# Kernel tuning notes

Hardware: AMD Instinct MI355X
Metric: run time of the kernel (lower is better)

Reference implementation:

```python
import jax, jax.numpy as jnp
import numpy as np
import math

NUM_HEADS = 12


def setup_inputs() -> dict:
    key = jax.random.key(0)
    ks = jax.random.split(key, 9)
    R, L, B, E = 128, 512, 1, 768
    s = 1.0 / math.sqrt(E)
    return {
        "x": jax.random.normal(ks[0], (R, L, B, E), dtype=jnp.float32),
        "wq": jax.random.normal(ks[1], (E, E), dtype=jnp.float32) * s,
        "bq": jax.random.normal(ks[2], (E,), dtype=jnp.float32) * 0.02,
        "wk": jax.random.normal(ks[3], (E, E), dtype=jnp.float32) * s,
        "bk": jax.random.normal(ks[4], (E,), dtype=jnp.float32) * 0.02,
        "wv": jax.random.normal(ks[5], (E, E), dtype=jnp.float32) * s,
        "bv": jax.random.normal(ks[6], (E,), dtype=jnp.float32) * 0.02,
        "wo": jax.random.normal(ks[7], (E, E), dtype=jnp.float32) * s,
        "bo": jax.random.normal(ks[8], (E,), dtype=jnp.float32) * 0.02,
    }


def reference(x, wq, bq, wk, bk, wv, bv, wo, bo):
    # x: [num_rows, num_cols, batch, embed_dim]
    R, L, B, E = x.shape
    H = NUM_HEADS
    D = E // H
    # scaling = head_dim**-0.5 / sqrt(num_rows)  (align_scaling)
    scaling = (D ** -0.5) / math.sqrt(R)

    q = (x @ wq.T + bq).reshape(R, L, B, H, D) * scaling
    k = (x @ wk.T + bk).reshape(R, L, B, H, D)
    v = (x @ wv.T + bv).reshape(R, L, B, H, D)

    # row attention: contract over rows r and head_dim d -> logits [h, n, i, j]
    attn_weights = jnp.einsum("rinhd,rjnhd->hnij", q, k)
    attn_probs = jax.nn.softmax(attn_weights, axis=-1)

    context = jnp.einsum("hnij,rjnhd->rinhd", attn_probs, v)
    context = context.reshape(R, L, B, E)
    output = context @ wo.T + bo
    return (output, attn_probs)
```

## Files before the change

kernel.cpp:

```cpp
#include <hip/hip_runtime.h>
#include <hip/hip_bf16.h>

typedef unsigned short u16;
typedef u16   u16x4 __attribute__((ext_vector_type(4)));
typedef u16   u16x8 __attribute__((ext_vector_type(8)));
typedef short bf16x8 __attribute__((ext_vector_type(8)));
typedef float f32x4 __attribute__((ext_vector_type(4)));

#define R_    128
#define L_    512
#define E_    768
#define H_    12
#define RD_   8192
#define M_    65536
#define OUT0_N 50331648
#define PART_ 3145728

__device__ __forceinline__ u16 rne_bf16(float f) {
  unsigned u = __builtin_bit_cast(unsigned, f);
  u += 0x7FFFu + ((u >> 16) & 1u);
  return (u16)(u >> 16);
}

__device__ __forceinline__ void gload_lds16(const u16* g, u16* l) {
  __builtin_amdgcn_global_load_lds(
      (const __attribute__((address_space(1))) void*)g,
      (__attribute__((address_space(3))) void*)l, 16, 0, 0);
}

__device__ __forceinline__ int xcd_remap(int d, int nwg) {
  return (d & 7) * (nwg >> 3) + (d >> 3);
}

__device__ __forceinline__ void gemm_core256(
    const u16* __restrict__ Ab, const u16* __restrict__ Bb,
    const int lda, const int ldb, const int K,
    u16* sm, f32x4 acc[8][4])
{
  const int t    = threadIdx.x;
  const int lane = t & 63;
  const int w    = t >> 6;
  const int wm   = (w >> 2) << 7;
  const int wn   = (w & 3) << 6;
  const int frow = lane & 15;

  const int srow  = t >> 2;
  const int gslot = (t & 3) ^ ((t >> 3) & 3);
  const u16* gA0 = Ab + (size_t)srow * lda + (gslot << 3);
  const u16* gA1 = Ab + (size_t)(srow + 128) * lda + (gslot << 3);
  const u16* gB0 = Bb + (size_t)srow * ldb + (gslot << 3);
  const u16* gB1 = Bb + (size_t)(srow + 128) * ldb + (gslot << 3);
  const int stg = t << 3;

  const int rdoff = (((lane >> 4) ^ ((lane >> 1) & 3)) << 3);

#define STAGE256(tt_, buf_)                                            \
  {                                                                    \
    const size_t ko_ = (size_t)(tt_) << 5;                             \
    gload_lds16(gA0 + ko_, (buf_) + stg);                              \
    gload_lds16(gA1 + ko_, (buf_) + 4096 + stg);                       \
    gload_lds16(gB0 + ko_, (buf_) + 8192 + stg);                       \
    gload_lds16(gB1 + ko_, (buf_) + 12288 + stg);                      \
  }

  const int nt = K >> 5;
  STAGE256(0, sm);
  if (nt > 1) STAGE256(1, sm + 16384);
  asm volatile("s_waitcnt vmcnt(4)" ::: "memory");
  __builtin_amdgcn_s_barrier();

  for (int tt = 0; tt < nt; ++tt) {
    u16* bufc = sm + (tt % 3) * 16384;
    const bool st = (tt + 2 < nt);
    if (st) STAGE256(tt + 2, sm + ((tt + 2) % 3) * 16384);

    bf16x8 af[8], bff[4];
#pragma unroll
    for (int b = 0; b < 4; ++b)
      bff[b] = *(const bf16x8*)(bufc + 8192 + ((wn + b * 16 + frow) << 5) + rdoff);
#pragma unroll
    for (int a = 0; a < 8; ++a)
      af[a] = *(const bf16x8*)(bufc + ((wm + a * 16 + frow) << 5) + rdoff);

    __builtin_amdgcn_s_setprio(1);
#pragma unroll
    for (int a = 0; a < 8; ++a)
#pragma unroll
      for (int b = 0; b < 4; ++b)
        acc[a][b] = __builtin_amdgcn_mfma_f32_16x16x32_bf16(af[a], bff[b], acc[a][b], 0, 0, 0);
    __builtin_amdgcn_s_setprio(0);

    if (st) asm volatile("s_waitcnt vmcnt(4)" ::: "memory");
    else    asm volatile("s_waitcnt vmcnt(0)" ::: "memory");
    __builtin_amdgcn_s_barrier();
  }
#undef STAGE256
}

#define EPILOGUE_IDX256                           \
  const int lane = threadIdx.x & 63;              \
  const int w    = threadIdx.x >> 6;              \
  const int wm   = (w >> 2) << 7;                 \
  const int wn   = (w & 3) << 6;                  \
  const int row4 = (lane >> 4) << 2;              \
  const int coll = lane & 15;

#define ACC_INIT256                               \
  f32x4 acc[8][4];                                \
  {                                               \
    f32x4 zz = {0.0f, 0.0f, 0.0f, 0.0f};          \
    _Pragma("unroll")                             \
    for (int a = 0; a < 8; ++a)                   \
      _Pragma("unroll")                           \
      for (int b = 0; b < 4; ++b) acc[a][b] = zz; \
  }

__device__ __forceinline__ void gemm_core(
    const u16* __restrict__ Ab, const u16* __restrict__ Bb,
    const int lda, const int ldb, const int K,
    u16* sm, f32x4 acc[4][4])
{
  const int t    = threadIdx.x;
  const int lane = t & 63;
  const int w    = t >> 6;
  const int wm   = (w >> 1) << 6;
  const int wn   = (w & 1) << 6;
  const int frow = lane & 15;

  const int srow = (w << 3) + (lane >> 3);
  const int scol = ((lane & 7) ^ (lane >> 3)) << 3;
  const u16* gA = Ab + (size_t)srow * lda + scol;
  const u16* gB = Bb + (size_t)srow * ldb + scol;
  const int stg_l = (w << 9) + (lane << 3);

#pragma unroll
  for (int j = 0; j < 4; ++j) {
    gload_lds16(gA + (size_t)(j << 5) * lda, sm + (j << 11) + stg_l);
    gload_lds16(gB + (size_t)(j << 5) * ldb, sm + 8192 + (j << 11) + stg_l);
  }

  const int nt = K >> 6;
  for (int tt = 0; tt < nt; ++tt) {
    const int cur = tt & 1;
    u16* bufc = sm + (cur << 14);
    u16* bufn = sm + ((cur ^ 1) << 14);
    __builtin_amdgcn_s_barrier();
    if (tt + 1 < nt) {
      const u16* gA1 = gA + ((size_t)(tt + 1) << 6);
      const u16* gB1 = gB + ((size_t)(tt + 1) << 6);
#pragma unroll
      for (int j = 0; j < 4; ++j) {
        gload_lds16(gA1 + (size_t)(j << 5) * lda, bufn + (j << 11) + stg_l);
        gload_lds16(gB1 + (size_t)(j << 5) * ldb, bufn + 8192 + (j << 11) + stg_l);
      }
      asm volatile("s_waitcnt vmcnt(8)" ::: "memory");
    } else {
      asm volatile("s_waitcnt vmcnt(0)" ::: "memory");
    }
    __builtin_amdgcn_s_barrier();
    const u16* sA = bufc;
    const u16* sB = bufc + 8192;
#pragma unroll
    for (int kk = 0; kk < 2; ++kk) {
      const int rdcol = (((kk << 2) + (lane >> 4)) ^ (lane & 7)) << 3;
      bf16x8 af[4], bff[4];
#pragma unroll
      for (int a = 0; a < 4; ++a)
        af[a] = *(const bf16x8*)(sA + ((wm + a * 16 + frow) << 6) + rdcol);
#pragma unroll
      for (int b = 0; b < 4; ++b)
        bff[b] = *(const bf16x8*)(sB + ((wn + b * 16 + frow) << 6) + rdcol);
#pragma unroll
      for (int a = 0; a < 4; ++a)
#pragma unroll
        for (int b = 0; b < 4; ++b)
          acc[a][b] = __builtin_amdgcn_mfma_f32_16x16x32_bf16(af[a], bff[b], acc[a][b], 0, 0, 0);
    }
  }
}

#define EPILOGUE_IDX                              \
  const int lane = threadIdx.x & 63;              \
  const int w    = threadIdx.x >> 6;              \
  const int wm   = (w >> 1) << 6;                 \
  const int wn   = (w & 1) << 6;                  \
  const int row4 = (lane >> 4) << 2;              \
  const int coll = lane & 15;

#define ACC_INIT                                  \
  f32x4 acc[4][4];                                \
  {                                               \
    f32x4 zz = {0.0f, 0.0f, 0.0f, 0.0f};          \
    _Pragma("unroll")                             \
    for (int a = 0; a < 4; ++a)                   \
      _Pragma("unroll")                           \
      for (int b = 0; b < 4; ++b) acc[a][b] = zz; \
  }

__global__ __launch_bounds__(512) void k_gemm_qkv(
    const u16* __restrict__ xbf, const u16* __restrict__ wqkv,
    const float* __restrict__ bq, const float* __restrict__ bk,
    const float* __restrict__ bv,
    u16* __restrict__ qt, u16* __restrict__ kt, u16* __restrict__ vt2,
    const float scaling)
{
  __shared__ __align__(16) u16 smem[49152];
  const int d0 = blockIdx.x + 9 * blockIdx.y;
  const int l  = xcd_remap(d0, 2304);
  const int bn = l % 9;
  const int bm = l / 9;
  ACC_INIT256;
  gemm_core256(xbf + (size_t)bm * 256 * E_, wqkv + (size_t)bn * 256 * E_,
               E_, E_, E_, smem, acc);
  EPILOGUE_IDX256;
  const int which = bn / 3;
  const int c0 = (bn % 3) << 8;
  const float* bias = (which == 0) ? bq : (which == 1) ? bk : bv;

  if (which < 2) {
    u16* dst = (which == 0) ? qt : kt;
    const float mult = (which == 0) ? scaling : 1.0f;
#pragma unroll
    for (int a = 0; a < 8; ++a) {
#pragma unroll
      for (int b = 0; b < 4; ++b) {
        const int c = c0 + wn + b * 16 + coll;
        const int h = c >> 6, d = c & 63;
        const float bias_v = bias[c];
#pragma unroll
        for (int r = 0; r < 4; ++r) {
          const int m = (bm << 8) + wm + a * 16 + row4 + r;
          const int rr = m >> 9, i = m & 511;
          const float v = (acc[a][b][r] + bias_v) * mult;
          dst[((size_t)(h * 512 + i) << 13) + (rr << 6) + d] = rne_bf16(v);
        }
      }
    }
  } else {
    const int rr = bm >> 1;
    const int j0 = (bm & 1) << 8;
    const int wc2 = (w & 3) >> 1;
    for (int p = 0; p < 2; ++p) {
      __syncthreads();
      if (wc2 == p) {
#pragma unroll
        for (int a = 0; a < 8; ++a) {
          const int ml = wm + a * 16 + row4;
#pragma unroll
          for (int b = 0; b < 4; ++b) {
            const int c = c0 + wn + b * 16 + coll;
            const int nl = (wn + b * 16 + coll) - (p << 7);
            const float bias_v = bias[c];
            u16x4 pk;
#pragma unroll
            for (int r = 0; r < 4; ++r) pk[r] = rne_bf16(acc[a][b][r] + bias_v);
            *(u16x4*)(smem + nl * 264 + ml) = pk;
          }
        }
      }
      __syncthreads();
      for (int idx = threadIdx.x; idx < 4096; idx += 512) {
        const int nl = idx >> 5, seg = idx & 31;
        const int c = c0 + (p << 7) + nl;
        const int h = c >> 6, d = c & 63;
        u16x8 vdat = *(const u16x8*)(smem + nl * 264 + (seg << 3));
        *(u16x8*)(vt2 + ((size_t)((h << 13) + (rr << 6) + d) << 9) + j0 + (seg << 3)) = vdat;
      }
    }
  }
}

__global__ __launch_bounds__(256) void k_gemm_logits(
    const u16* __restrict__ qt, const u16* __restrict__ kt,
    float* __restrict__ lgp)
{
  __shared__ __align__(16) u16 smem[32768];
  const int d0 = blockIdx.x + 4 * blockIdx.y + 16 * blockIdx.z;
  const int l  = xcd_remap(d0, 768);
  const int bm = l & 3, bn = (l >> 2) & 3;
  const int hk = l >> 4;
  const int h  = hk >> 2, ks = hk & 3;
  ACC_INIT;
  const u16* A = qt + ((size_t)h << 22) + ((size_t)bm << 20) + (ks << 11);
  const u16* B = kt + ((size_t)h << 22) + ((size_t)bn << 20) + (ks << 11);
  gemm_core(A, B, RD_, RD_, 2048, smem, acc);
  EPILOGUE_IDX;
  float* dst = lgp + ((size_t)(ks * 12 + h) << 18);
#pragma unroll
  for (int a = 0; a < 4; ++a)
#pragma unroll
    for (int b = 0; b < 4; ++b) {
      const int j = bn * 128 + wn + b * 16 + coll;
#pragma unroll
      for (int r = 0; r < 4; ++r) {
        const int i = bm * 128 + wm + a * 16 + row4 + r;
        dst[((size_t)i << 9) + j] = acc[a][b][r];
      }
    }
}

__global__ __launch_bounds__(256) void k_softmax(
    const float* __restrict__ lgp, float* __restrict__ probs,
    u16* __restrict__ pbf)
{
  const int row = blockIdx.x;
  const size_t base = (size_t)row << 9;
  const int t = threadIdx.x;
  const int lane = t & 63, w = t >> 6;
  float x0 = (lgp[base + t]       + lgp[PART_ + base + t])
           + (lgp[2 * (size_t)PART_ + base + t]       + lgp[3 * (size_t)PART_ + base + t]);
  float x1 = (lgp[base + t + 256] + lgp[PART_ + base + t + 256])
           + (lgp[2 * (size_t)PART_ + base + t + 256] + lgp[3 * (size_t)PART_ + base + t + 256]);
  float m = fmaxf(x0, x1);
#pragma unroll
  for (int off = 32; off > 0; off >>= 1) m = fmaxf(m, __shfl_xor(m, off, 64));
  __shared__ float red[8];
  if (lane == 0) red[w] = m;
  __syncthreads();
  m = fmaxf(fmaxf(red[0], red[1]), fmaxf(red[2], red[3]));
  float e0 = __expf(x0 - m), e1 = __expf(x1 - m);
  float s = e0 + e1;
#pragma unroll
  for (int off = 32; off > 0; off >>= 1) s += __shfl_xor(s, off, 64);
  if (lane == 0) red[4 + w] = s;
  __syncthreads();
  s = (red[4] + red[5]) + (red[6] + red[7]);
  const float inv = 1.0f / s;
  const float p0 = e0 * inv, p1 = e1 * inv;
  probs[base + t] = p0;
  probs[base + t + 256] = p1;
  pbf[base + t]       = rne_bf16(p0);
  pbf[base + t + 256] = rne_bf16(p1);
}

__global__ __launch_bounds__(512) void k_gemm_ctx(
    const u16* __restrict__ pbf, const u16* __restrict__ vt2,
    u16* __restrict__ ctx)
{
  __shared__ __align__(16) u16 smem[49152];
  const int d0 = blockIdx.x + (blockIdx.y << 6);
  const int l  = xcd_remap(d0, 768);
  const int bm = l & 1, bn = (l >> 1) & 31, h = l >> 6;
  ACC_INIT256;
  const u16* A = pbf + ((size_t)h << 18) + ((size_t)bm << 17);
  const u16* B = vt2 + ((size_t)h << 22) + ((size_t)bn << 17);
  gemm_core256(A, B, 512, 512, 512, smem, acc);
  EPILOGUE_IDX256;
#pragma unroll
  for (int a = 0; a < 8; ++a)
#pragma unroll
    for (int b = 0; b < 4; ++b) {
      const int n = (bn << 8) + wn + b * 16 + coll;
      const int rr = n >> 6, d = n & 63;
#pragma unroll
      for (int r = 0; r < 4; ++r) {
        const int i = (bm << 8) + wm + a * 16 + row4 + r;
        ctx[(size_t)((rr << 9) + i) * E_ + (h << 6) + d] = rne_bf16(acc[a][b][r]);
      }
    }
}

__global__ __launch_bounds__(512) void k_gemm_out(
    const u16* __restrict__ ctx, const u16* __restrict__ wob,
    const float* __restrict__ bo, float* __restrict__ out0)
{
  __shared__ __align__(16) u16 smem[49152];
  const int d0 = blockIdx.x + 3 * blockIdx.y;
  const int l  = xcd_remap(d0, 768);
  const int bn = l % 3;
  const int bm = l / 3;
  ACC_INIT256;
  gemm_core256(ctx + (size_t)bm * 256 * E_, wob + (size_t)bn * 256 * E_,
               E_, E_, E_, smem, acc);
  EPILOGUE_IDX256;
#pragma unroll
  for (int a = 0; a < 8; ++a)
#pragma unroll
    for (int b = 0; b < 4; ++b) {
      const int n = (bn << 8) + wn + b * 16 + coll;
      const float bias_v = bo[n];
#pragma unroll
      for (int r = 0; r < 4; ++r) {
        const int m = (bm << 8) + wm + a * 16 + row4 + r;
        out0[(size_t)m * E_ + n] = acc[a][b][r] + bias_v;
      }
    }
}

__device__ __forceinline__ u16x4 cvt4(float4 v) {
  u16x4 o;
  o.x = rne_bf16(v.x); o.y = rne_bf16(v.y);
  o.z = rne_bf16(v.z); o.w = rne_bf16(v.w);
  return o;
}

__global__ __launch_bounds__(256) void k_cvt_x(
    const float4* __restrict__ src, u16x4* __restrict__ dst, const int n4)
{
  const int stride = gridDim.x * blockDim.x;
  for (int i = blockIdx.x * blockDim.x + threadIdx.x; i < n4; i += stride)
    dst[i] = cvt4(src[i]);
}

__global__ __launch_bounds__(256) void k_cvt_w(
    const float4* __restrict__ wq, const float4* __restrict__ wk,
    const float4* __restrict__ wv, const float4* __restrict__ wo,
    u16x4* __restrict__ wqkv, u16x4* __restrict__ wob)
{
  const int n4 = (E_ * E_) / 4;
  const int stride = gridDim.x * blockDim.x;
  for (int i = blockIdx.x * blockDim.x + threadIdx.x; i < n4; i += stride) {
    wqkv[i]            = cvt4(wq[i]);
    wqkv[n4 + i]       = cvt4(wk[i]);
    wqkv[2 * n4 + i]   = cvt4(wv[i]);
    wob[i]             = cvt4(wo[i]);
  }
}

__global__ void k_ws_too_small(float* out0) {
  if (threadIdx.x == 0 && blockIdx.x == 0) out0[0] = 1.0e9f;
}

extern "C" void kernel_launch(void* const* d_in, const int* in_sizes, int n_in,
                              void* d_out, int out_size, void* d_ws, size_t ws_size,
                              hipStream_t stream)
{
  const float* x  = (const float*)d_in[0];
  const float* wq = (const float*)d_in[1];
  const float* bq = (const float*)d_in[2];
  const float* wk = (const float*)d_in[3];
  const float* bk = (const float*)d_in[4];
  const float* wv = (const float*)d_in[5];
  const float* bv = (const float*)d_in[6];
  const float* wo = (const float*)d_in[7];
  const float* bo = (const float*)d_in[8];

  float* out0 = (float*)d_out;
  float* outp = out0 + (size_t)OUT0_N;

  const size_t off_xbf   = 0;
  const size_t off_qt    = 100663296;
  const size_t off_kt    = 201326592;
  const size_t off_vt    = 301989888;
  const size_t off_pbf   = 402653184;
  const size_t off_wqkv  = 408944640;
  const size_t off_wob   = 412483584;
  const size_t need      = 413663232;

  if (ws_size < need) {
    k_ws_too_small<<<1, 64, 0, stream>>>(out0);
    return;
  }

  char* ws = (char*)d_ws;
  u16* xbf  = (u16*)(ws + off_xbf);
  float* lgp = (float*)(ws + off_xbf);
  u16* qt   = (u16*)(ws + off_qt);
  u16* kt   = (u16*)(ws + off_kt);
  u16* vt2  = (u16*)(ws + off_vt);
  u16* pbf  = (u16*)(ws + off_pbf);
  u16* wqkv = (u16*)(ws + off_wqkv);
  u16* wob  = (u16*)(ws + off_wob);

  const float scaling = 0.011048543456039806f;

  k_cvt_x<<<2048, 256, 0, stream>>>((const float4*)x, (u16x4*)xbf, OUT0_N / 4);
  k_cvt_w<<<192, 256, 0, stream>>>((const float4*)wq, (const float4*)wk,
                                   (const float4*)wv, (const float4*)wo,
                                   (u16x4*)wqkv, (u16x4*)wob);
  k_gemm_qkv<<<dim3(9, 256), 512, 0, stream>>>(xbf, wqkv, bq, bk, bv,
                                               qt, kt, vt2, scaling);
  k_gemm_logits<<<dim3(4, 4, 48), 256, 0, stream>>>(qt, kt, lgp);
  k_softmax<<<6144, 256, 0, stream>>>(lgp, outp, pbf);
  k_gemm_ctx<<<dim3(64, 12), 512, 0, stream>>>(pbf, vt2, xbf );
  k_gemm_out<<<dim3(3, 256), 512, 0, stream>>>(xbf, wob, bo, out0);
}
```

Before: 617.8 us.

## Split GEMM main loop into two half-phases interleaving global loads with MFMA

Restructures the bf16 GEMM mainloop so each K-step runs two phases of 16 MFMAs. The A and B prefetches for tile tt+2 are spread across those phases, along with the LDS fragment loads, in a ping-pong style with extra barriers. Fragment registers drop from 8 to 4 for A. The aim is to overlap memory issue with matrix compute more evenly and reduce register pressure, but it adds four barriers per iteration in place of one.

Result: no change. 611.8 us (-1.0%).

```diff
diff --git a/kernel.cpp b/kernel.cpp
--- a/kernel.cpp
+++ b/kernel.cpp
@@ -54,47 +54,67 @@
 
   const int rdoff = (((lane >> 4) ^ ((lane >> 1) & 3)) << 3);
 
-#define STAGE256(tt_, buf_)                                            \
-  {                                                                    \
-    const size_t ko_ = (size_t)(tt_) << 5;                             \
-    gload_lds16(gA0 + ko_, (buf_) + stg);                              \
-    gload_lds16(gA1 + ko_, (buf_) + 4096 + stg);                       \
-    gload_lds16(gB0 + ko_, (buf_) + 8192 + stg);                       \
-    gload_lds16(gB1 + ko_, (buf_) + 12288 + stg);                      \
-  }
-
   const int nt = K >> 5;
-  STAGE256(0, sm);
-  if (nt > 1) STAGE256(1, sm + 16384);
+  gload_lds16(gA0, sm + stg);
+  gload_lds16(gA1, sm + 4096 + stg);
+  gload_lds16(gB0, sm + 8192 + stg);
+  gload_lds16(gB1, sm + 12288 + stg);
+  if (nt > 1) {
+    u16* b1 = sm + 16384;
+    gload_lds16(gA0 + 32, b1 + stg);
+    gload_lds16(gA1 + 32, b1 + 4096 + stg);
+    gload_lds16(gB0 + 32, b1 + 8192 + stg);
+    gload_lds16(gB1 + 32, b1 + 12288 + stg);
+  }
   asm volatile("s_waitcnt vmcnt(4)" ::: "memory");
   __builtin_amdgcn_s_barrier();
 
   for (int tt = 0; tt < nt; ++tt) {
     u16* bufc = sm + (tt % 3) * 16384;
+    u16* bufn = sm + ((tt + 2) % 3) * 16384;
     const bool st = (tt + 2 < nt);
-    if (st) STAGE256(tt + 2, sm + ((tt + 2) % 3) * 16384);
-
-    bf16x8 af[8], bff[4];
+    const size_t ko = (size_t)(tt + 2) << 5;
+
+    bf16x8 af[4], bff[4];
 #pragma unroll
     for (int b = 0; b < 4; ++b)
       bff[b] = *(const bf16x8*)(bufc + 8192 + ((wn + b * 16 + frow) << 5) + rdoff);
 #pragma unroll
-    for (int a = 0; a < 8; ++a)
+    for (int a = 0; a < 4; ++a)
       af[a] = *(const bf16x8*)(bufc + ((wm + a * 16 + frow) << 5) + rdoff);
-
+    if (st) {
+      gload_lds16(gA0 + ko, bufn + stg);
+      gload_lds16(gA1 + ko, bufn + 4096 + stg);
+    }
+    __builtin_amdgcn_s_barrier();
     __builtin_amdgcn_s_setprio(1);
 #pragma unroll
-    for (int a = 0; a < 8; ++a)
+    for (int a = 0; a < 4; ++a)
 #pragma unroll
       for (int b = 0; b < 4; ++b)
         acc[a][b] = __builtin_amdgcn_mfma_f32_16x16x32_bf16(af[a], bff[b], acc[a][b], 0, 0, 0);
     __builtin_amdgcn_s_setprio(0);
-
-    if (st) asm volatile("s_waitcnt vmcnt(4)" ::: "memory");
-    else    asm volatile("s_waitcnt vmcnt(0)" ::: "memory");
-    __builtin_amdgcn_s_barrier();
-  }
-#undef STAGE256
+    __builtin_amdgcn_s_barrier();
+#pragma unroll
+    for (int a = 0; a < 4; ++a)
+      af[a] = *(const bf16x8*)(bufc + ((wm + (a + 4) * 16 + frow) << 5) + rdoff);
+    if (st) {
+      gload_lds16(gB0 + ko, bufn + 8192 + stg);
+      gload_lds16(gB1 + ko, bufn + 12288 + stg);
+      asm volatile("s_waitcnt vmcnt(4)" ::: "memory");
+    } else {
+      asm volatile("s_waitcnt vmcnt(0)" ::: "memory");
+    }
+    __builtin_amdgcn_s_barrier();
+    __builtin_amdgcn_s_setprio(1);
+#pragma unroll
+    for (int a = 0; a < 4; ++a)
+#pragma unroll
+      for (int b = 0; b < 4; ++b)
+        acc[a + 4][b] = __builtin_amdgcn_mfma_f32_16x16x32_bf16(af[a], bff[b], acc[a + 4][b], 0, 0, 0);
+    __builtin_amdgcn_s_setprio(0);
+    __builtin_amdgcn_s_barrier();
+  }
 }
 
 #define EPILOGUE_IDX256                           \
```
